# Optimization experiments

Measured on AMD Instinct MI355X. Metric: run time of the kernel, lower is better.

## Reference

```python
import jax, jax.numpy as jnp
import numpy as np

POLY_DEGREE = 3


def setup_inputs() -> dict:
    key = jax.random.key(0)
    k1, k2, k3 = jax.random.split(key, 3)
    B, L, D = 8192, 16, 4096
    total = sum(L ** d for d in range(POLY_DEGREE + 1))  # 4369
    z = jax.random.normal(k1, (B, L), dtype=jnp.float32)
    W = jax.random.normal(k2, (total, D), dtype=jnp.float32) * 0.02
    b = jax.random.normal(k3, (D,), dtype=jnp.float32) * 0.02
    return {"z": z, "W": W, "b": b}


def poly_features(z):
    # Batched equivalent of per-sample torch.kron chain:
    # degree 0 -> [1]; degree k -> kron(deg_{k-1} feature, z) per sample.
    B = z.shape[0]
    feats = [jnp.ones((B, 1), dtype=z.dtype)]
    cur = z  # degree 1
    feats.append(cur)
    for _ in range(2, POLY_DEGREE + 1):
        # kron(out, latent): (i, j) -> out_i * latent_j
        cur = (cur[:, :, None] * z[:, None, :]).reshape(B, -1)
        feats.append(cur)
    return jnp.concatenate(feats, axis=1)  # [B, total_poly_terms]


def reference(z, W, b):
    x = poly_features(z)          # [B, T]
    return x @ W + b              # [B, data_dim]
```

## Files before the change

kernel.cpp:

```cpp
#include <hip/hip_runtime.h>
#include <hip/hip_bf16.h>

#define NDIM  4096
#define MROWS 8192
#define PREAL 969
#define KP    1024
#define NT    16
#define NWFOLD 1024

typedef unsigned short u16;
typedef __attribute__((ext_vector_type(8))) __bf16 bf16x8;
typedef __attribute__((ext_vector_type(8))) u16 u16x8;
typedef __attribute__((ext_vector_type(4))) float f32x4;

__device__ __forceinline__ u16 bf16rne(float f) {
  unsigned int u = __builtin_bit_cast(unsigned int, f);
  u += 0x7fffu + ((u >> 16) & 1u);
  return (u16)(u >> 16);
}

struct Tbl { int v[KP]; };
constexpr Tbl make_table() {
  Tbl t{};
  for (int p = 0; p < KP; ++p) t.v[p] = -1;
  int p = 0;
  t.v[p++] = (16 << 10) | (16 << 5) | 16;
  for (int i = 0; i < 16; ++i) t.v[p++] = (i << 10) | (16 << 5) | 16;
  for (int i = 0; i < 16; ++i)
    for (int j = i; j < 16; ++j) t.v[p++] = (i << 10) | (j << 5) | 16;
  for (int i = 0; i < 16; ++i)
    for (int j = i; j < 16; ++j)
      for (int k = j; k < 16; ++k) t.v[p++] = (i << 10) | (j << 5) | k;
  return t;
}
__device__ constexpr Tbl TBL = make_table();

__global__ void prep_kernel(const float* __restrict__ z, const float* __restrict__ W,
                            const float* __restrict__ bias,
                            u16* __restrict__ xb, u16* __restrict__ wfbt) {
  __shared__ float tile[64][65];
  __shared__ float zs[17];
  const int bx = blockIdx.x;
  const int tid = threadIdx.x;

  if (bx < NWFOLD) {
    const int p0 = (bx & 15) * 64;
    const int d0 = (bx >> 4) * 64;
    const int d4 = (tid & 15) * 4;
    const int rb = tid >> 4;
    const int dd = d0 + d4;
#pragma unroll
    for (int pp = 0; pp < 4; ++pp) {
      const int r = pp * 16 + rb;
      const int p = p0 + r;
      const int enc = TBL.v[p];
      f32x4 v = {0.f, 0.f, 0.f, 0.f};
      if (enc >= 0) {
        const int i = enc >> 10, j = (enc >> 5) & 31, k = enc & 31;
        if (k == 16) {
          if (j == 16) {
            if (i == 16) {
              v = *reinterpret_cast<const f32x4*>(W + dd);
              f32x4 bb = *reinterpret_cast<const f32x4*>(bias + dd);
              v.x += bb.x; v.y += bb.y; v.z += bb.z; v.w += bb.w;
            } else {
              v = *reinterpret_cast<const f32x4*>(W + (size_t)(1 + i) * NDIM + dd);
            }
          } else {
            v = *reinterpret_cast<const f32x4*>(W + (size_t)(17 + i * 16 + j) * NDIM + dd);
            if (i != j) {
              f32x4 w2 = *reinterpret_cast<const f32x4*>(W + (size_t)(17 + j * 16 + i) * NDIM + dd);
              v.x += w2.x; v.y += w2.y; v.z += w2.z; v.w += w2.w;
            }
          }
        } else {
          int rows[6];
          int nr = 0;
          rows[nr++] = 273 + i * 256 + j * 16 + k;
          if (i == j && j == k) {
          } else if (i == j) {
            rows[nr++] = 273 + i * 256 + k * 16 + i;
            rows[nr++] = 273 + k * 256 + i * 16 + i;
          } else if (j == k) {
            rows[nr++] = 273 + j * 256 + i * 16 + j;
            rows[nr++] = 273 + j * 256 + j * 16 + i;
          } else {
            rows[nr++] = 273 + i * 256 + k * 16 + j;
            rows[nr++] = 273 + j * 256 + i * 16 + k;
            rows[nr++] = 273 + j * 256 + k * 16 + i;
            rows[nr++] = 273 + k * 256 + i * 16 + j;
            rows[nr++] = 273 + k * 256 + j * 16 + i;
          }
          v = *reinterpret_cast<const f32x4*>(W + (size_t)rows[0] * NDIM + dd);
          for (int s = 1; s < nr; ++s) {
            f32x4 w2 = *reinterpret_cast<const f32x4*>(W + (size_t)rows[s] * NDIM + dd);
            v.x += w2.x; v.y += w2.y; v.z += w2.z; v.w += w2.w;
          }
        }
      }
#pragma unroll
      for (int jj = 0; jj < 4; ++jj) tile[r][d4 + jj] = v[jj];
    }
    __syncthreads();
#pragma unroll
    for (int round = 0; round < 2; ++round) {
      const int v = round * 256 + tid;
      const int d = v >> 3;
      const int tg = v & 7;
      u16x8 pack;
#pragma unroll
      for (int e = 0; e < 8; ++e) pack[e] = bf16rne(tile[tg * 8 + e][d]);
      *reinterpret_cast<u16x8*>(wfbt + (size_t)(d0 + d) * KP + p0 + tg * 8) = pack;
    }
  } else {
    const int row = bx - NWFOLD;
    if (tid < 16) zs[tid] = z[row * 16 + tid];
    if (tid == 16) zs[16] = 1.0f;
    __syncthreads();
    u16* xrow = xb + (size_t)row * KP;
    for (int g = tid; g < KP / 8; g += 256) {
      u16x8 pack;
#pragma unroll
      for (int e = 0; e < 8; ++e) {
        const int enc = TBL.v[g * 8 + e];
        float v = 0.0f;
        if (enc >= 0) v = zs[enc >> 10] * (zs[(enc >> 5) & 31] * zs[enc & 31]);
        pack[e] = bf16rne(v);
      }
      *reinterpret_cast<u16x8*>(xrow + g * 8) = pack;
    }
  }
}

#define GLOAD(gp, lp)                                                                     \
  __builtin_amdgcn_global_load_lds((const __attribute__((address_space(1))) unsigned int*)(gp), \
                                   (__attribute__((address_space(3))) unsigned int*)(lp), 16, 0, 0)

__device__ __forceinline__ void bar() {
  asm volatile("" ::: "memory");
  __builtin_amdgcn_s_barrier();
  asm volatile("" ::: "memory");
}

#define VM4 asm volatile("s_waitcnt vmcnt(4)" ::: "memory")
#define VM2 asm volatile("s_waitcnt vmcnt(2)" ::: "memory")
#define VM0 asm volatile("s_waitcnt vmcnt(0)" ::: "memory")

__global__ __launch_bounds__(512, 2) void gemm_kernel(const u16* __restrict__ xb,
                                                      const u16* __restrict__ wbt,
                                                      float* __restrict__ out) {
  __shared__ u16 lds[2 * 32768];

  const int bid  = blockIdx.x;
  const int xcd  = bid & 7;
  const int idx  = bid >> 3;
  const int mtl  = (idx >> 3) & 3;
  const int ntl  = (idx & 7) | ((idx >> 5) << 3);
  const int brow = (xcd * 4 + mtl) * 256;
  const int bcol = ntl * 256;

  const int tid  = threadIdx.x;
  const int lane = tid & 63;
  const int wid  = tid >> 6;
  const int wr   = wid >> 2;
  const int wc   = wid & 3;
  const int f    = lane & 15;
  const int q    = lane >> 4;
  const int f7   = f & 7;

  const int lr = lane >> 3;
  const int swzc = ((lane & 7) ^ lr) * 8;
  const u16* gA = xb  + (size_t)(brow + lr) * KP + swzc;
  const u16* gB = wbt + (size_t)(bcol + lr) * KP + swzc;
  const int aB0 = (wid >> 2) * 128 + (wid & 3) * 16;
  const int bB0 = (wid >> 1) * 64 + (wid & 1) * 16;

#define STGQ(gptr, region, rb, U) do {                                               \
    GLOAD((gptr) + (size_t)(rb) * KP + (U) * 64, (region) + (rb) * 64);              \
    GLOAD((gptr) + (size_t)((rb) + 8) * KP + (U) * 64, (region) + ((rb) + 8) * 64);  \
  } while (0)

#define RD_A(mi, kk) (*reinterpret_cast<const bf16x8*>(bufA + (wr * 128 + (mi) * 16 + f) * 64 + (((kk) * 4 + q) ^ f7) * 8))
#define RD_B(ni, kk) (*reinterpret_cast<const bf16x8*>(bufB + (wc * 64 + (ni) * 16 + f) * 64 + (((kk) * 4 + q) ^ f7) * 8))

#define RDA4(MOFF) do {                                                              \
    _Pragma("unroll") for (int _i = 0; _i < 4; ++_i) {                               \
      a_[_i][0] = RD_A((MOFF) + _i, 0); a_[_i][1] = RD_A((MOFF) + _i, 1); }          \
  } while (0)
#define RDB2(NOFF) do {                                                              \
    _Pragma("unroll") for (int _i = 0; _i < 2; ++_i) {                               \
      b_[(NOFF) + _i][0] = RD_B((NOFF) + _i, 0); b_[(NOFF) + _i][1] = RD_B((NOFF) + _i, 1); } \
  } while (0)

#define QUAD(MOFF, NOFF) do {                                                        \
    __builtin_amdgcn_s_setprio(1);                                                   \
    _Pragma("unroll") for (int _m = 0; _m < 4; ++_m)                                 \
    _Pragma("unroll") for (int _n = 0; _n < 2; ++_n)                                 \
    _Pragma("unroll") for (int _k = 0; _k < 2; ++_k)                                 \
      acc[(MOFF) + _m][(NOFF) + _n] = __builtin_amdgcn_mfma_f32_16x16x32_bf16(       \
          a_[_m][_k], b_[(NOFF) + _n][_k], acc[(MOFF) + _m][(NOFF) + _n], 0, 0, 0);  \
    __builtin_amdgcn_s_setprio(0);                                                   \
  } while (0)

#define TILE_BODY(cA, cB, nA, nB, U) do {                                            \
    bufA = (cA); bufB = (cB);                                                        \
    RDA4(0); RDB2(0); STGQ(gA, (nA), aB0, (U));                                      \
    QUAD(0, 0); VM4; bar();                                                          \
    RDB2(2);          STGQ(gB, (nB), bB0, (U));                                      \
    QUAD(0, 2); VM4; bar();                                                          \
    RDA4(4);          STGQ(gB, (nB), bB0 + 32, (U));                                 \
    QUAD(4, 2); bar();                                                               \
                      STGQ(gA, (nA), aB0 + 64, (U));                                 \
    QUAD(4, 0); VM4; bar();                                                          \
  } while (0)

#define TILE_LAST(cA, cB) do {                                                       \
    bufA = (cA); bufB = (cB);                                                        \
    RDA4(0); RDB2(0);                                                                \
    QUAD(0, 0); VM2; bar();                                                          \
    RDB2(2);                                                                         \
    QUAD(0, 2); VM0; bar();                                                          \
    RDA4(4);                                                                         \
    QUAD(4, 2); bar();                                                               \
    QUAD(4, 0);                                                                      \
  } while (0)

  f32x4 acc[8][4] = {};
  bf16x8 a_[4][2], b_[4][2];
  const u16 *bufA, *bufB;

  u16* b0A = lds;            u16* b0B = lds + 16384;
  u16* b1A = lds + 32768;    u16* b1B = b1A + 16384;

  STGQ(gA, b0A, aB0, 0); STGQ(gB, b0B, bB0, 0);
  STGQ(gB, b0B, bB0 + 32, 0); STGQ(gA, b0A, aB0 + 64, 0);
  VM4; bar();

  for (int t = 0; t < NT - 2; t += 2) {
    TILE_BODY(b0A, b0B, b1A, b1B, t + 1);
    TILE_BODY(b1A, b1B, b0A, b0B, t + 2);
  }
  TILE_BODY(b0A, b0B, b1A, b1B, NT - 1);
  TILE_LAST(b1A, b1B);

  const int r0 = brow + wr * 128 + q * 4;
  const int c0 = bcol + wc * 64 + f;
#pragma unroll
  for (int mi = 0; mi < 8; ++mi)
#pragma unroll
    for (int ni = 0; ni < 4; ++ni) {
#pragma unroll
      for (int j = 0; j < 4; ++j)
        out[(size_t)(r0 + mi * 16 + j) * NDIM + (c0 + ni * 16)] = acc[mi][ni][j];
    }
}

__global__ void fallback_kernel(const float* __restrict__ z, const float* __restrict__ W,
                                const float* __restrict__ bias, float* __restrict__ out) {
  __shared__ float feat[4369];
  const int row = blockIdx.x;
  const int tid = threadIdx.x;
  for (int t = tid; t < 4369; t += 256) {
    float v;
    if (t == 0) v = 1.0f;
    else if (t < 17) v = z[row * 16 + t - 1];
    else if (t < 273) { int u = t - 17; v = z[row * 16 + (u >> 4)] * z[row * 16 + (u & 15)]; }
    else { int u = t - 273; v = z[row * 16 + ((u >> 8) & 15)] * (z[row * 16 + ((u >> 4) & 15)] * z[row * 16 + (u & 15)]); }
    feat[t] = v;
  }
  __syncthreads();
  float acc[16];
#pragma unroll
  for (int j = 0; j < 16; ++j) acc[j] = bias[tid + 256 * j];
  for (int t = 0; t < 4369; ++t) {
    const float fv = feat[t];
    const float* wrow = W + (size_t)t * NDIM;
#pragma unroll
    for (int j = 0; j < 16; ++j) acc[j] = fmaf(fv, wrow[tid + 256 * j], acc[j]);
  }
  float* orow = out + (size_t)row * NDIM;
#pragma unroll
  for (int j = 0; j < 16; ++j) orow[tid + 256 * j] = acc[j];
}

extern "C" void kernel_launch(void* const* d_in, const int* in_sizes, int n_in,
                              void* d_out, int out_size, void* d_ws, size_t ws_size,
                              hipStream_t stream) {
  const float* z = (const float*)d_in[0];
  const float* W = (const float*)d_in[1];
  const float* b = (const float*)d_in[2];
  float* out = (float*)d_out;

  const size_t xb_elems  = (size_t)MROWS * KP;
  const size_t wbt_elems = (size_t)NDIM * KP;
  const size_t need = (xb_elems + wbt_elems) * sizeof(u16);

  if (ws_size >= need) {
    u16* xb  = (u16*)d_ws;
    u16* wbt = xb + xb_elems;
    prep_kernel<<<NWFOLD + MROWS, 256, 0, stream>>>(z, W, b, xb, wbt);
    gemm_kernel<<<(MROWS / 256) * (NDIM / 256), 512, 0, stream>>>(xb, wbt, out);
  } else {
    fallback_kernel<<<MROWS, 256, 0, stream>>>(z, W, b, out);
  }
}
```

Baseline: 106.2 us.

## Shrink GEMM block tile to 128x128 with 4 waves and windowed block mapping

Reduces the GEMM block tile from 256x256 (8 waves) to 128x128 (4 waves). Each wave now computes 64x64 instead of 128x64, and LDS per block drops to 64 KB double-buffered. The block-to-tile mapping becomes an XCD-aware windowed layout for L2 reuse, and extra barriers are placed before each MFMA group. This gives more blocks (2048) for better load balance and occupancy, at the cost of lower arithmetic intensity per block and more global loads per FLOP.

```diff
diff --git a/kernel.cpp b/kernel.cpp
--- a/kernel.cpp
+++ b/kernel.cpp
@@ -146,24 +146,26 @@
 #define VM2 asm volatile("s_waitcnt vmcnt(2)" ::: "memory")
 #define VM0 asm volatile("s_waitcnt vmcnt(0)" ::: "memory")
 
-__global__ __launch_bounds__(512, 2) void gemm_kernel(const u16* __restrict__ xb,
+__global__ __launch_bounds__(256, 2) void gemm_kernel(const u16* __restrict__ xb,
                                                       const u16* __restrict__ wbt,
                                                       float* __restrict__ out) {
-  __shared__ u16 lds[2 * 32768];
+  __shared__ u16 lds[2 * 16384];
 
   const int bid  = blockIdx.x;
   const int xcd  = bid & 7;
   const int idx  = bid >> 3;
-  const int mtl  = (idx >> 3) & 3;
-  const int ntl  = (idx & 7) | ((idx >> 5) << 3);
-  const int brow = (xcd * 4 + mtl) * 256;
-  const int bcol = ntl * 256;
+  const int win  = idx >> 5;
+  const int w    = idx & 31;
+  const int mtl  = (win >> 2) * 4 + (w >> 3);
+  const int ntl  = (win & 3) * 8 + (w & 7);
+  const int brow = (xcd * 8 + mtl) * 128;
+  const int bcol = ntl * 128;
 
   const int tid  = threadIdx.x;
   const int lane = tid & 63;
   const int wid  = tid >> 6;
-  const int wr   = wid >> 2;
-  const int wc   = wid & 3;
+  const int wr   = wid >> 1;
+  const int wc   = wid & 1;
   const int f    = lane & 15;
   const int q    = lane >> 4;
   const int f7   = f & 7;
@@ -172,68 +174,67 @@
   const int swzc = ((lane & 7) ^ lr) * 8;
   const u16* gA = xb  + (size_t)(brow + lr) * KP + swzc;
   const u16* gB = wbt + (size_t)(bcol + lr) * KP + swzc;
-  const int aB0 = (wid >> 2) * 128 + (wid & 3) * 16;
-  const int bB0 = (wid >> 1) * 64 + (wid & 1) * 16;
+  const int qB0 = (wid >> 1) * 64 + (wid & 1) * 16;
 
 #define STGQ(gptr, region, rb, U) do {                                               \
     GLOAD((gptr) + (size_t)(rb) * KP + (U) * 64, (region) + (rb) * 64);              \
     GLOAD((gptr) + (size_t)((rb) + 8) * KP + (U) * 64, (region) + ((rb) + 8) * 64);  \
   } while (0)
 
-#define RD_A(mi, kk) (*reinterpret_cast<const bf16x8*>(bufA + (wr * 128 + (mi) * 16 + f) * 64 + (((kk) * 4 + q) ^ f7) * 8))
+#define RD_A(mi, kk) (*reinterpret_cast<const bf16x8*>(bufA + (wr * 64 + (mi) * 16 + f) * 64 + (((kk) * 4 + q) ^ f7) * 8))
 #define RD_B(ni, kk) (*reinterpret_cast<const bf16x8*>(bufB + (wc * 64 + (ni) * 16 + f) * 64 + (((kk) * 4 + q) ^ f7) * 8))
 
-#define RDA4(MOFF) do {                                                              \
-    _Pragma("unroll") for (int _i = 0; _i < 4; ++_i) {                               \
-      a_[_i][0] = RD_A((MOFF) + _i, 0); a_[_i][1] = RD_A((MOFF) + _i, 1); }          \
-  } while (0)
-#define RDB2(NOFF) do {                                                              \
-    _Pragma("unroll") for (int _i = 0; _i < 2; ++_i) {                               \
-      b_[(NOFF) + _i][0] = RD_B((NOFF) + _i, 0); b_[(NOFF) + _i][1] = RD_B((NOFF) + _i, 1); } \
-  } while (0)
-
-#define QUAD(MOFF, NOFF) do {                                                        \
+#define RDA2(i0) do {                                                                \
+    a_[i0][0] = RD_A((i0), 0);     a_[i0][1] = RD_A((i0), 1);                        \
+    a_[(i0)+1][0] = RD_A((i0)+1, 0); a_[(i0)+1][1] = RD_A((i0)+1, 1);                \
+  } while (0)
+#define RDB2(i0) do {                                                                \
+    b_[i0][0] = RD_B((i0), 0);     b_[i0][1] = RD_B((i0), 1);                        \
+    b_[(i0)+1][0] = RD_B((i0)+1, 0); b_[(i0)+1][1] = RD_B((i0)+1, 1);                \
+  } while (0)
+
+#define OCT(M0, N0) do {                                                             \
     __builtin_amdgcn_s_setprio(1);                                                   \
-    _Pragma("unroll") for (int _m = 0; _m < 4; ++_m)                                 \
+    _Pragma("unroll") for (int _m = 0; _m < 2; ++_m)                                 \
     _Pragma("unroll") for (int _n = 0; _n < 2; ++_n)                                 \
     _Pragma("unroll") for (int _k = 0; _k < 2; ++_k)                                 \
-      acc[(MOFF) + _m][(NOFF) + _n] = __builtin_amdgcn_mfma_f32_16x16x32_bf16(       \
-          a_[_m][_k], b_[(NOFF) + _n][_k], acc[(MOFF) + _m][(NOFF) + _n], 0, 0, 0);  \
+      acc[(M0) + _m][(N0) + _n] = __builtin_amdgcn_mfma_f32_16x16x32_bf16(           \
+          a_[(M0) + _m][_k], b_[(N0) + _n][_k], acc[(M0) + _m][(N0) + _n], 0, 0, 0); \
     __builtin_amdgcn_s_setprio(0);                                                   \
   } while (0)
 
 #define TILE_BODY(cA, cB, nA, nB, U) do {                                            \
     bufA = (cA); bufB = (cB);                                                        \
-    RDA4(0); RDB2(0); STGQ(gA, (nA), aB0, (U));                                      \
-    QUAD(0, 0); VM4; bar();                                                          \
-    RDB2(2);          STGQ(gB, (nB), bB0, (U));                                      \
-    QUAD(0, 2); VM4; bar();                                                          \
-    RDA4(4);          STGQ(gB, (nB), bB0 + 32, (U));                                 \
-    QUAD(4, 2); bar();                                                               \
-                      STGQ(gA, (nA), aB0 + 64, (U));                                 \
-    QUAD(4, 0); VM4; bar();                                                          \
+    RDA2(0); RDB2(0); STGQ(gA, (nA), qB0, (U));                                      \
+    bar(); OCT(0, 0); VM4; bar();                                                    \
+    RDB2(2);          STGQ(gB, (nB), qB0, (U));                                      \
+    bar(); OCT(0, 2); VM4; bar();                                                    \
+    RDA2(2);          STGQ(gB, (nB), qB0 + 32, (U));                                 \
+    bar(); OCT(2, 2); bar();                                                         \
+                      STGQ(gA, (nA), qB0 + 32, (U));                                 \
+    bar(); OCT(2, 0); VM4; bar();                                                    \
   } while (0)
 
 #define TILE_LAST(cA, cB) do {                                                       \
     bufA = (cA); bufB = (cB);                                                        \
-    RDA4(0); RDB2(0);                                                                \
-    QUAD(0, 0); VM2; bar();                                                          \
+    RDA2(0); RDB2(0);                                                                \
+    bar(); OCT(0, 0); VM2; bar();                                                    \
     RDB2(2);                                                                         \
-    QUAD(0, 2); VM0; bar();                                                          \
-    RDA4(4);                                                                         \
-    QUAD(4, 2); bar();                                                               \
-    QUAD(4, 0);                                                                      \
-  } while (0)
-
-  f32x4 acc[8][4] = {};
+    bar(); OCT(0, 2); VM0; bar();                                                    \
+    RDA2(2);                                                                         \
+    bar(); OCT(2, 2); bar();                                                         \
+    OCT(2, 0);                                                                       \
+  } while (0)
+
+  f32x4 acc[4][4] = {};
   bf16x8 a_[4][2], b_[4][2];
   const u16 *bufA, *bufB;
 
-  u16* b0A = lds;            u16* b0B = lds + 16384;
-  u16* b1A = lds + 32768;    u16* b1B = b1A + 16384;
-
-  STGQ(gA, b0A, aB0, 0); STGQ(gB, b0B, bB0, 0);
-  STGQ(gB, b0B, bB0 + 32, 0); STGQ(gA, b0A, aB0 + 64, 0);
+  u16* b0A = lds;            u16* b0B = lds + 8192;
+  u16* b1A = lds + 16384;    u16* b1B = b1A + 8192;
+
+  STGQ(gA, b0A, qB0, 0); STGQ(gB, b0B, qB0, 0);
+  STGQ(gB, b0B, qB0 + 32, 0); STGQ(gA, b0A, qB0 + 32, 0);
   VM4; bar();
 
   for (int t = 0; t < NT - 2; t += 2) {
@@ -243,10 +244,10 @@
   TILE_BODY(b0A, b0B, b1A, b1B, NT - 1);
   TILE_LAST(b1A, b1B);
 
-  const int r0 = brow + wr * 128 + q * 4;
+  const int r0 = brow + wr * 64 + q * 4;
   const int c0 = bcol + wc * 64 + f;
 #pragma unroll
-  for (int mi = 0; mi < 8; ++mi)
+  for (int mi = 0; mi < 4; ++mi)
 #pragma unroll
     for (int ni = 0; ni < 4; ++ni) {
 #pragma unroll
@@ -299,7 +300,7 @@
     u16* xb  = (u16*)d_ws;
     u16* wbt = xb + xb_elems;
     prep_kernel<<<NWFOLD + MROWS, 256, 0, stream>>>(z, W, b, xb, wbt);
-    gemm_kernel<<<(MROWS / 256) * (NDIM / 256), 512, 0, stream>>>(xb, wbt, out);
+    gemm_kernel<<<(MROWS / 128) * (NDIM / 128), 256, 0, stream>>>(xb, wbt, out);
   } else {
     fallback_kernel<<<MROWS, 256, 0, stream>>>(z, W, b, out);
   }
```

Result: no change. 104.2 us (-1.9%).
